# Kernel tuning notes

Hardware: AMD Instinct MI355X
Metric: run time of the kernel (lower is better)

Reference implementation:

```python
import jax, jax.numpy as jnp
import numpy as np

VOCAB, HID, L, HEADS, INTER, MAXSEQ, NCLS = 30522, 128, 2, 2, 512, 512, 2
HEAD = HID // HEADS
B, S = 128, 512


def _tlin(x, W, b):
    # TernaryLinear: threshold-quantize W to {-1,0,1} with per-tensor scale,
    # then ordinary linear. delta = 0.7*mean|W|, alpha = mean|W| over kept entries.
    absW = jnp.abs(W)
    delta = 0.7 * jnp.mean(absW)
    mask = (absW > delta).astype(W.dtype)
    alpha = jnp.sum(absW * mask) / jnp.maximum(jnp.sum(mask), 1.0)
    Wq = jnp.sign(W) * mask * alpha  # [out, in]
    return jnp.einsum('...i,oi->...o', x, Wq) + b


def _ln(x, g, b, eps=1e-5):
    m = jnp.mean(x, axis=-1, keepdims=True)
    v = jnp.var(x, axis=-1, keepdims=True)
    return (x - m) * jax.lax.rsqrt(v + eps) * g + b


def setup_inputs() -> dict:
    key = jax.random.key(0)
    ks = iter(jax.random.split(key, 64))
    n = lambda shape, s=0.02: jax.random.normal(next(ks), shape, dtype=jnp.float32) * s
    inp = {
        'input_ids': jax.random.randint(next(ks), (B, S), 0, VOCAB, dtype=jnp.int32).astype(jnp.int64),
        'tok_emb': n((VOCAB, HID)),
        'pos_emb': n((MAXSEQ, HID)),
        'ln_g': jnp.ones((HID,), jnp.float32), 'ln_b': jnp.zeros((HID,), jnp.float32),
        'qw': n((L, HID, HID)), 'qb': jnp.zeros((L, HID), jnp.float32),
        'kw': n((L, HID, HID)), 'kb': jnp.zeros((L, HID), jnp.float32),
        'vw': n((L, HID, HID)), 'vb': jnp.zeros((L, HID), jnp.float32),
        'aow': n((L, HID, HID)), 'aob': jnp.zeros((L, HID), jnp.float32),
        'iw': n((L, INTER, HID)), 'ib': jnp.zeros((L, INTER), jnp.float32),
        'fow': n((L, HID, INTER)), 'fob': jnp.zeros((L, HID), jnp.float32),
        'ln1g': jnp.ones((L, HID), jnp.float32), 'ln1b': jnp.zeros((L, HID), jnp.float32),
        'ln2g': jnp.ones((L, HID), jnp.float32), 'ln2b': jnp.zeros((L, HID), jnp.float32),
        'clf_w': n((NCLS, HID)), 'clf_b': jnp.zeros((NCLS,), jnp.float32),
    }
    return inp


def reference(input_ids, tok_emb, pos_emb, ln_g, ln_b, qw, qb, kw, kb, vw, vb,
              aow, aob, iw, ib, fow, fob, ln1g, ln1b, ln2g, ln2b, clf_w, clf_b):
    b, s = input_ids.shape
    x = tok_emb[input_ids] + pos_emb[jnp.arange(s)][None, :, :]  # [B,S,H]
    x = _ln(x, ln_g, ln_b)
    scale = 1.0 / (HEAD ** 0.5)
    for l in range(L):
        q = _tlin(x, qw[l], qb[l]).reshape(b, s, HEADS, HEAD)
        k = _tlin(x, kw[l], kb[l]).reshape(b, s, HEADS, HEAD)
        v = _tlin(x, vw[l], vb[l]).reshape(b, s, HEADS, HEAD)
        scores = jnp.einsum('bqhd,bkhd->bhqk', q, k) * scale
        attn = jax.nn.softmax(scores, axis=-1)
        ctx = jnp.einsum('bhqk,bkhd->bqhd', attn, v).reshape(b, s, HID)
        attn_out = _tlin(ctx, aow[l], aob[l])
        x = _ln(x + attn_out, ln1g[l], ln1b[l])
        ff = _tlin(jax.nn.relu(_tlin(x, iw[l], ib[l])), fow[l], fob[l])
        x = _ln(x + ff, ln2g[l], ln2b[l])
    cls = x[:, 0, :]
    logits = _tlin(cls, clf_w, clf_b)  # [B, NCLS]
    return logits
```

## Files before the change

### kernel.cpp

```cpp
#include <hip/hip_runtime.h>

typedef short bf8s __attribute__((ext_vector_type(8)));
typedef float f32x4 __attribute__((ext_vector_type(4)));

#define MFMA16(a, b, c) __builtin_amdgcn_mfma_f32_16x16x32_bf16(a, b, c, 0, 0, 0)

constexpr int S_ = 512, HID_ = 128, B_ = 128, M_ = B_ * S_;

__device__ inline short f2bf(float f) {
  unsigned u = __float_as_uint(f);
  u = (u + 0x7fffu + ((u >> 16) & 1u)) >> 16;
  return (short)u;
}
__device__ inline float bf2f(short s) {
  return __uint_as_float(((unsigned)(unsigned short)s) << 16);
}

__device__ inline float block_red1024(float v, float* red) {
  #pragma unroll
  for (int m = 32; m >= 1; m >>= 1) v += __shfl_xor(v, m);
  __syncthreads();
  if ((threadIdx.x & 63) == 0) red[threadIdx.x >> 6] = v;
  __syncthreads();
  float t = 0.f;
  #pragma unroll
  for (int i = 0; i < 16; ++i) t += red[i];
  return t;
}

__device__ inline void mat_info(int mat, const float* qw, const float* kw,
                                const float* vw, const float* aow, const float* iw,
                                const float* fw, const float* cw,
                                const float** src, int* n, int* doff) {
  if (mat < 6) {
    int l = mat / 3, which = mat % 3;
    const float* t[3] = {qw, kw, vw};
    *src = t[which] + l * 16384; *n = 16384; *doff = l * 49152 + which * 16384;
  } else if (mat < 8) {
    int l = mat - 6;
    *src = aow + l * 16384; *n = 16384; *doff = 98304 + l * 16384;
  } else if (mat < 10) {
    *src = iw + (mat - 8) * 65536; *n = 65536; *doff = 131072 + (mat - 8) * 65536;
  } else if (mat < 12) {
    *src = fw + (mat - 10) * 65536; *n = 65536; *doff = 262144 + (mat - 10) * 65536;
  } else {
    *src = cw; *n = 256; *doff = 393216;
  }
}

__global__ __launch_bounds__(1024) void k_qe(const float* qw, const float* kw,
    const float* vw, const float* aow, const float* iw, const float* fw,
    const float* cw, short* WQ,
    const int* __restrict__ ids, const float* __restrict__ tok,
    const float* __restrict__ pos, const float* __restrict__ g,
    const float* __restrict__ bb, short* xb) {
  __shared__ float red[16];
  int tid = threadIdx.x;
  if (blockIdx.x < 13) {
    const float* src; int n, doff;
    mat_info(blockIdx.x, qw, kw, vw, aow, iw, fw, cw, &src, &n, &doff);
    float s = 0.f;
    for (int i = tid; i < n; i += 1024) s += fabsf(src[i]);
    s = block_red1024(s, red);
    float delta = 0.7f * s / (float)n;
    float s2 = 0.f, c2 = 0.f;
    for (int i = tid; i < n; i += 1024) {
      float a = fabsf(src[i]);
      if (a > delta) { s2 += a; c2 += 1.f; }
    }
    s2 = block_red1024(s2, red);
    c2 = block_red1024(c2, red);
    float alpha = s2 / fmaxf(c2, 1.f);
    for (int i = tid; i < n; i += 1024) {
      float w = src[i];
      WQ[doff + i] = (fabsf(w) > delta) ? f2bf(w > 0.f ? alpha : -alpha) : (short)0;
    }
  } else {
    int wave = tid >> 6, lane = tid & 63;
    int t = (blockIdx.x - 13) * 16 + wave;
    int s = t & (S_ - 1);
    int id = ids[t];
    float e0 = tok[(size_t)id * HID_ + lane] + pos[(size_t)s * HID_ + lane];
    float e1 = tok[(size_t)id * HID_ + 64 + lane] + pos[(size_t)s * HID_ + 64 + lane];
    float sum = e0 + e1, ssq = e0 * e0 + e1 * e1;
    #pragma unroll
    for (int m = 32; m >= 1; m >>= 1) {
      sum += __shfl_xor(sum, m);
      ssq += __shfl_xor(ssq, m);
    }
    float mean = sum / 128.f;
    float var = ssq / 128.f - mean * mean;
    float rs = rsqrtf(var + 1e-5f);
    size_t o = (size_t)t * HID_;
    xb[o + lane]      = f2bf((e0 - mean) * rs * g[lane] + bb[lane]);
    xb[o + 64 + lane] = f2bf((e1 - mean) * rs * g[64 + lane] + bb[64 + lane]);
  }
}

__global__ __launch_bounds__(256) void k_qkv(
    const short* __restrict__ A, const short* __restrict__ W,
    const float* __restrict__ b0, const float* __restrict__ b1,
    const float* __restrict__ b2, short* outb) {
  __shared__ short Wl[128 * 136];
  int tid = threadIdx.x, lane = tid & 63, wave = tid >> 6;
  int row16 = lane & 15, quad = lane >> 4;
  int tok0 = blockIdx.x * 64 + wave * 16;
  int nbase = blockIdx.y * 128;

  const short* arow = A + (size_t)(tok0 + row16) * 128 + quad * 8;
  bf8s av[4];
  #pragma unroll
  for (int ki = 0; ki < 4; ++ki) av[ki] = *(const bf8s*)(arow + ki * 32);

  {
    int r = tid >> 1, half = tid & 1;
    const short* src = W + (size_t)(nbase + r) * 128 + half * 64;
    short* dst = &Wl[r * 136 + half * 64];
    #pragma unroll
    for (int j = 0; j < 8; ++j)
      *(bf8s*)(dst + j * 8) = *(const bf8s*)(src + j * 8);
  }
  __syncthreads();

  f32x4 acc[8] = {};
  #pragma unroll
  for (int ki = 0; ki < 4; ++ki)
    #pragma unroll
    for (int ot = 0; ot < 8; ++ot) {
      bf8s b = *(const bf8s*)(&Wl[(ot * 16 + row16) * 136 + ki * 32 + quad * 8]);
      acc[ot] = MFMA16(av[ki], b, acc[ot]);
    }

  const float* bp = (blockIdx.y == 0) ? b0 : ((blockIdx.y == 1) ? b1 : b2);
  float osc = (blockIdx.y == 0) ? 0.125f : 1.0f;
  int m0 = tok0 + quad * 4;
  #pragma unroll
  for (int ot = 0; ot < 8; ++ot) {
    int col = ot * 16 + row16;
    float bi = bp[col];
    #pragma unroll
    for (int r = 0; r < 4; ++r) {
      float v = (acc[ot][r] + bi) * osc;
      outb[(size_t)(m0 + r) * 384 + nbase + col] = f2bf(v);
    }
  }
}

__global__ __launch_bounds__(256) void k_aoff(
    const short* __restrict__ cb, const short* __restrict__ Wa,
    const float* __restrict__ aob, const float* __restrict__ ln1g,
    const float* __restrict__ ln1b, const short* __restrict__ Wi,
    const short* __restrict__ Wf, const float* __restrict__ ib,
    const float* __restrict__ fb, const float* __restrict__ ln2g,
    const float* __restrict__ ln2b, short* xb) {
  __shared__ short SM[22528];
  int tid = threadIdx.x, lane = tid & 63, wave = tid >> 6;
  int row16 = lane & 15, quad = lane >> 4;
  int tok0 = blockIdx.x * 64 + wave * 16;
  int m0 = tok0 + quad * 4;

  const short* arow = cb + (size_t)(tok0 + row16) * 128 + quad * 8;
  bf8s av[4];
  #pragma unroll
  for (int ki = 0; ki < 4; ++ki) av[ki] = *(const bf8s*)(arow + ki * 32);

  {
    int r = tid >> 1, half = tid & 1;
    const short* src = Wa + (size_t)r * 128 + half * 64;
    short* dst = &SM[r * 136 + half * 64];
    #pragma unroll
    for (int j = 0; j < 8; ++j)
      *(bf8s*)(dst + j * 8) = *(const bf8s*)(src + j * 8);
  }
  __syncthreads();

  f32x4 acc[8] = {};
  #pragma unroll
  for (int ki = 0; ki < 4; ++ki)
    #pragma unroll
    for (int ot = 0; ot < 8; ++ot) {
      bf8s b = *(const bf8s*)(&SM[(ot * 16 + row16) * 136 + ki * 32 + quad * 8]);
      acc[ot] = MFMA16(av[ki], b, acc[ot]);
    }

  int rwi = tid >> 2, q4 = tid & 3;
  int rwf = tid >> 1, hwf = tid & 1;
  const short* wisrc = Wi + (size_t)rwi * HID_ + q4 * 32;
  const short* wfsrc = Wf + (size_t)rwf * 512 + hwf * 32;
  bf8s wiR[4], wfR[4];
  #pragma unroll
  for (int j = 0; j < 4; ++j) {
    wiR[j] = *(const bf8s*)(wisrc + j * 8);
    wfR[j] = *(const bf8s*)(wfsrc + j * 8);
  }

  {
    float sum[4] = {}, ssq[4] = {};
    #pragma unroll
    for (int ot = 0; ot < 8; ++ot) {
      int col = ot * 16 + row16;
      float bi = aob[col];
      #pragma unroll
      for (int r = 0; r < 4; ++r) {
        float v = acc[ot][r] + bi + bf2f(xb[(size_t)(m0 + r) * HID_ + col]);
        acc[ot][r] = v;
        sum[r] += v; ssq[r] += v * v;
      }
    }
    #pragma unroll
    for (int m = 1; m <= 8; m <<= 1)
      #pragma unroll
      for (int r = 0; r < 4; ++r) {
        sum[r] += __shfl_xor(sum[r], m);
        ssq[r] += __shfl_xor(ssq[r], m);
      }
    float mean[4], rstd[4];
    #pragma unroll
    for (int r = 0; r < 4; ++r) {
      mean[r] = sum[r] / 128.f;
      float var = ssq[r] / 128.f - mean[r] * mean[r];
      rstd[r] = rsqrtf(var + 1e-5f);
    }
    #pragma unroll
    for (int ot = 0; ot < 8; ++ot) {
      int col = ot * 16 + row16;
      float gg = ln1g[col], bb2 = ln1b[col];
      #pragma unroll
      for (int r = 0; r < 4; ++r)
        acc[ot][r] = (acc[ot][r] - mean[r]) * rstd[r] * gg + bb2;
    }
  }

  #pragma unroll
  for (int ot = 0; ot < 8; ++ot) {
    int col = ot * 16 + row16;
    #pragma unroll
    for (int r = 0; r < 4; ++r)
      xb[(size_t)(m0 + r) * HID_ + col] = f2bf(acc[ot][r]);
  }

  __syncthreads();
  short* myX = &SM[wave * 4352];
  #pragma unroll
  for (int ot = 0; ot < 8; ++ot)
    #pragma unroll
    for (int r = 0; r < 4; ++r)
      myX[(quad * 4 + r) * 136 + ot * 16 + row16] = f2bf(acc[ot][r]);
  #pragma unroll
  for (int ki = 0; ki < 4; ++ki)
    av[ki] = *(const bf8s*)(myX + row16 * 136 + ki * 32 + quad * 8);

  short* SWi = SM;
  short* SWf = SM + 8704;
  short* mySt = SM + 17920 + wave * 1152;
  f32x4 acc2[8] = {};
  for (int c = 0; c < 8; ++c) {
    __syncthreads();
    {
      short* dwi = SWi + rwi * 136 + q4 * 32;
      short* dwf = SWf + rwf * 72 + hwf * 32;
      #pragma unroll
      for (int j = 0; j < 4; ++j) {
        *(bf8s*)(dwi + j * 8) = wiR[j];
        *(bf8s*)(dwf + j * 8) = wfR[j];
      }
    }
    __syncthreads();
    if (c < 7) {
      const short* ws1 = wisrc + (size_t)(c + 1) * 64 * HID_;
      const short* ws2 = wfsrc + (c + 1) * 64;
      #pragma unroll
      for (int j = 0; j < 4; ++j) {
        wiR[j] = *(const bf8s*)(ws1 + j * 8);
        wfR[j] = *(const bf8s*)(ws2 + j * 8);
      }
    }

    f32x4 hacc[4] = {};
    #pragma unroll
    for (int ki = 0; ki < 4; ++ki)
      #pragma unroll
      for (int ot = 0; ot < 4; ++ot) {
        bf8s b = *(const bf8s*)(SWi + (ot * 16 + row16) * 136 + ki * 32 + quad * 8);
        hacc[ot] = MFMA16(av[ki], b, hacc[ot]);
      }
    #pragma unroll
    for (int ot = 0; ot < 4; ++ot) {
      float bi = ib[c * 64 + ot * 16 + row16];
      #pragma unroll
      for (int r = 0; r < 4; ++r)
        mySt[(quad * 4 + r) * 72 + ot * 16 + row16] =
            f2bf(fmaxf(hacc[ot][r] + bi, 0.f));
    }
    bf8s ha0 = *(const bf8s*)(mySt + row16 * 72 + quad * 8);
    bf8s ha1 = *(const bf8s*)(mySt + row16 * 72 + 32 + quad * 8);
    #pragma unroll
    for (int ot = 0; ot < 8; ++ot) {
      bf8s bA = *(const bf8s*)(SWf + (ot * 16 + row16) * 72 + quad * 8);
      bf8s bB = *(const bf8s*)(SWf + (ot * 16 + row16) * 72 + 32 + quad * 8);
      acc2[ot] = MFMA16(ha0, bA, acc2[ot]);
      acc2[ot] = MFMA16(ha1, bB, acc2[ot]);
    }
  }

  float sum[4] = {}, ssq[4] = {};
  #pragma unroll
  for (int ot = 0; ot < 8; ++ot) {
    int col = ot * 16 + row16;
    float bi = fb[col];
    #pragma unroll
    for (int r = 0; r < 4; ++r) {
      float v = acc2[ot][r] + bi + bf2f(xb[(size_t)(m0 + r) * HID_ + col]);
      acc2[ot][r] = v;
      sum[r] += v; ssq[r] += v * v;
    }
  }
  #pragma unroll
  for (int m = 1; m <= 8; m <<= 1)
    #pragma unroll
    for (int r = 0; r < 4; ++r) {
      sum[r] += __shfl_xor(sum[r], m);
      ssq[r] += __shfl_xor(ssq[r], m);
    }
  float mean[4], rstd[4];
  #pragma unroll
  for (int r = 0; r < 4; ++r) {
    mean[r] = sum[r] / 128.f;
    float var = ssq[r] / 128.f - mean[r] * mean[r];
    rstd[r] = rsqrtf(var + 1e-5f);
  }
  #pragma unroll
  for (int ot = 0; ot < 8; ++ot) {
    int col = ot * 16 + row16;
    float gg = ln2g[col], bb2 = ln2b[col];
    #pragma unroll
    for (int r = 0; r < 4; ++r) {
      float v = (acc2[ot][r] - mean[r]) * rstd[r] * gg + bb2;
      xb[(size_t)(m0 + r) * HID_ + col] = f2bf(v);
    }
  }
}

__global__ __launch_bounds__(512) void k_attn(const short* __restrict__ qkv,
                                              short* __restrict__ O) {
  __shared__ short Kl[64 * 72];
  __shared__ short Vtl[64 * 72];
  __shared__ short Pl[8][16 * 72];

  int tid = threadIdx.x, lane = tid & 63, wave = tid >> 6;
  int row16 = lane & 15, quad = lane >> 4;
  int b = blockIdx.x >> 2, h = (blockIdx.x >> 1) & 1, qhalf = blockIdx.x & 1;
  const short* base  = qkv + (size_t)b * S_ * 384;
  const short* kbase = base + 128 + h * 64;
  const short* vbase = base + 256 + h * 64;
  int q0 = qhalf * 256 + wave * 32;

  bf8s qa[2][2];
  #pragma unroll
  for (int qf = 0; qf < 2; ++qf) {
    const short* qrow = base + h * 64 +
        (size_t)(q0 + qf * 16 + row16) * 384 + quad * 8;
    qa[qf][0] = *(const bf8s*)(qrow);
    qa[qf][1] = *(const bf8s*)(qrow + 32);
  }

  int krow = tid >> 3, dgk = tid & 7;
  int vkey = tid & 63, dgv = tid >> 6;
  const short* kptr = kbase + (size_t)krow * 384 + dgk * 8;
  const short* vptr = vbase + (size_t)vkey * 384 + dgv * 8;
  bf8s kst = *(const bf8s*)(kptr);
  bf8s vst = *(const bf8s*)(vptr);

  float li[2][4] = {};
  f32x4 oacc[2][4] = {};
  short* myP = &Pl[wave][0];

  for (int kt0 = 0; kt0 < S_; kt0 += 64) {
    if (kt0) __syncthreads();
    *(bf8s*)(&Kl[krow * 72 + dgk * 8]) = kst;
    #pragma unroll
    for (int j = 0; j < 8; ++j) Vtl[(dgv * 8 + j) * 72 + vkey] = vst[j];
    __syncthreads();
    if (kt0 + 64 < S_) {
      kst = *(const bf8s*)(kptr + (size_t)(kt0 + 64) * 384);
      vst = *(const bf8s*)(vptr + (size_t)(kt0 + 64) * 384);
    }

    f32x4 sc[2][4] = {};
    #pragma unroll
    for (int ks = 0; ks < 4; ++ks) {
      const short* kp = &Kl[(ks * 16 + row16) * 72 + quad * 8];
      bf8s k0 = *(const bf8s*)(kp);
      bf8s k1 = *(const bf8s*)(kp + 32);
      sc[0][ks] = MFMA16(qa[0][0], k0, sc[0][ks]);
      sc[0][ks] = MFMA16(qa[0][1], k1, sc[0][ks]);
      sc[1][ks] = MFMA16(qa[1][0], k0, sc[1][ks]);
      sc[1][ks] = MFMA16(qa[1][1], k1, sc[1][ks]);
    }

    #pragma unroll
    for (int qf = 0; qf < 2; ++qf) {
      #pragma unroll
      for (int ks = 0; ks < 4; ++ks)
        #pragma unroll
        for (int r = 0; r < 4; ++r) {
          float pv = __expf(sc[qf][ks][r]);
          li[qf][r] += pv;
          myP[(quad * 4 + r) * 72 + ks * 16 + row16] = f2bf(pv);
        }
      bf8s pa0 = *(const bf8s*)(&myP[row16 * 72 + quad * 8]);
      bf8s pa1 = *(const bf8s*)(&myP[row16 * 72 + 32 + quad * 8]);
      #pragma unroll
      for (int dt = 0; dt < 4; ++dt) {
        const short* vp = &Vtl[(dt * 16 + row16) * 72 + quad * 8];
        bf8s v0 = *(const bf8s*)(vp);
        bf8s v1 = *(const bf8s*)(vp + 32);
        oacc[qf][dt] = MFMA16(pa0, v0, oacc[qf][dt]);
        oacc[qf][dt] = MFMA16(pa1, v1, oacc[qf][dt]);
      }
    }
  }

  #pragma unroll
  for (int qf = 0; qf < 2; ++qf) {
    float inv[4];
    #pragma unroll
    for (int r = 0; r < 4; ++r) {
      float t = li[qf][r];
      #pragma unroll
      for (int m = 1; m <= 8; m <<= 1) t += __shfl_xor(t, m);
      inv[r] = 1.f / t;
    }
    size_t trow = (size_t)(b * S_ + q0 + qf * 16 + quad * 4);
    #pragma unroll
    for (int dt = 0; dt < 4; ++dt)
      #pragma unroll
      for (int r = 0; r < 4; ++r)
        O[(trow + r) * HID_ + h * 64 + dt * 16 + row16] =
            f2bf(oacc[qf][dt][r] * inv[r]);
  }
}

__global__ __launch_bounds__(256) void k_clf(const short* __restrict__ xb,
    const short* __restrict__ Wc, const float* __restrict__ cbias, float* out) {
  int i = threadIdx.x;
  int b = i >> 1, c = i & 1;
  float s = 0.f;
  for (int k = 0; k < HID_; ++k)
    s += bf2f(xb[(size_t)b * S_ * HID_ + k]) * bf2f(Wc[c * HID_ + k]);
  out[b * 2 + c] = s + cbias[c];
}

extern "C" void kernel_launch(void* const* d_in, const int* in_sizes, int n_in,
                              void* d_out, int out_size, void* d_ws, size_t ws_size,
                              hipStream_t stream) {
  const int*   ids     = (const int*)d_in[0];
  const float* tok_emb = (const float*)d_in[1];
  const float* pos_emb = (const float*)d_in[2];
  const float* ln_g    = (const float*)d_in[3];
  const float* ln_bb   = (const float*)d_in[4];
  const float* qw      = (const float*)d_in[5];
  const float* qbias   = (const float*)d_in[6];
  const float* kw      = (const float*)d_in[7];
  const float* kbias   = (const float*)d_in[8];
  const float* vw      = (const float*)d_in[9];
  const float* vbias   = (const float*)d_in[10];
  const float* aow     = (const float*)d_in[11];
  const float* aobias  = (const float*)d_in[12];
  const float* iw      = (const float*)d_in[13];
  const float* ibias   = (const float*)d_in[14];
  const float* fow     = (const float*)d_in[15];
  const float* fbias   = (const float*)d_in[16];
  const float* ln1g    = (const float*)d_in[17];
  const float* ln1b    = (const float*)d_in[18];
  const float* ln2g    = (const float*)d_in[19];
  const float* ln2b    = (const float*)d_in[20];
  const float* clfw    = (const float*)d_in[21];
  const float* clfb    = (const float*)d_in[22];

  char* ws = (char*)d_ws;
  short* WQ  = (short*)ws;
  short* xb  = (short*)(ws + 1048576);
  short* qkv = (short*)(ws + 1048576 + 16777216);
  short* cb_ = qkv + (size_t)M_ * 384;

  k_qe<<<13 + M_ / 16, 1024, 0, stream>>>(qw, kw, vw, aow, iw, fow, clfw, WQ,
                                          ids, tok_emb, pos_emb, ln_g, ln_bb, xb);

  for (int l = 0; l < 2; ++l) {
    const short* Wqkv = WQ + (size_t)l * 49152;
    const short* Wa   = WQ + 98304 + (size_t)l * 16384;
    const short* Wi   = WQ + 131072 + (size_t)l * 65536;
    const short* Wf   = WQ + 262144 + (size_t)l * 65536;

    k_qkv<<<dim3(M_ / 64, 3), 256, 0, stream>>>(
        xb, Wqkv, qbias + l * HID_, kbias + l * HID_, vbias + l * HID_, qkv);
    k_attn<<<512, 512, 0, stream>>>(qkv, cb_);
    k_aoff<<<M_ / 64, 256, 0, stream>>>(
        cb_, Wa, aobias + l * HID_, ln1g + l * HID_, ln1b + l * HID_,
        Wi, Wf, ibias + l * 512, fbias + l * HID_,
        ln2g + l * HID_, ln2b + l * HID_, xb);
  }

  k_clf<<<1, 256, 0, stream>>>(xb, WQ + 393216, clfb, (float*)d_out);
}
```

Before: 355.4 us.

## Fuse layer-1 QKV projection into layer-0 FFN kernel; use 128-token blocks

The layer-0 attention-output/FFN kernel now also computes the layer-1 QKV projection from its LayerNorm output, which removes one k_qkv launch and one re-read of the hidden state from global memory. Blocks now cover 128 tokens with 512 threads, so each weight tile staged in LDS is shared by twice as many tokens. The LDS row pitch changes from 136 to 144 (and 72 to 80), altering the bank-conflict pattern. In exchange, LDS use per block is higher and the fused kernel holds more registers, which may lower occupancy.

```diff
diff --git a/kernel.cpp b/kernel.cpp
--- a/kernel.cpp
+++ b/kernel.cpp
@@ -101,7 +101,7 @@
     const short* __restrict__ A, const short* __restrict__ W,
     const float* __restrict__ b0, const float* __restrict__ b1,
     const float* __restrict__ b2, short* outb) {
-  __shared__ short Wl[128 * 136];
+  __shared__ short Wl[128 * 144];
   int tid = threadIdx.x, lane = tid & 63, wave = tid >> 6;
   int row16 = lane & 15, quad = lane >> 4;
   int tok0 = blockIdx.x * 64 + wave * 16;
@@ -115,7 +115,7 @@
   {
     int r = tid >> 1, half = tid & 1;
     const short* src = W + (size_t)(nbase + r) * 128 + half * 64;
-    short* dst = &Wl[r * 136 + half * 64];
+    short* dst = &Wl[r * 144 + half * 64];
     #pragma unroll
     for (int j = 0; j < 8; ++j)
       *(bf8s*)(dst + j * 8) = *(const bf8s*)(src + j * 8);
@@ -127,7 +127,7 @@
   for (int ki = 0; ki < 4; ++ki)
     #pragma unroll
     for (int ot = 0; ot < 8; ++ot) {
-      bf8s b = *(const bf8s*)(&Wl[(ot * 16 + row16) * 136 + ki * 32 + quad * 8]);
+      bf8s b = *(const bf8s*)(&Wl[(ot * 16 + row16) * 144 + ki * 32 + quad * 8]);
       acc[ot] = MFMA16(av[ki], b, acc[ot]);
     }
 
@@ -146,17 +146,21 @@
   }
 }
 
-__global__ __launch_bounds__(256) void k_aoff(
+template <int DOQKV>
+__global__ __launch_bounds__(512) void k_aoff(
     const short* __restrict__ cb, const short* __restrict__ Wa,
     const float* __restrict__ aob, const float* __restrict__ ln1g,
     const float* __restrict__ ln1b, const short* __restrict__ Wi,
     const short* __restrict__ Wf, const float* __restrict__ ib,
     const float* __restrict__ fb, const float* __restrict__ ln2g,
-    const float* __restrict__ ln2b, short* xb) {
-  __shared__ short SM[22528];
+    const float* __restrict__ ln2b, short* xb,
+    const short* __restrict__ Wqkv2, const float* __restrict__ qb2,
+    const float* __restrict__ kb2, const float* __restrict__ vb2,
+    short* qkvout) {
+  __shared__ short SM[29696];
   int tid = threadIdx.x, lane = tid & 63, wave = tid >> 6;
   int row16 = lane & 15, quad = lane >> 4;
-  int tok0 = blockIdx.x * 64 + wave * 16;
+  int tok0 = blockIdx.x * 128 + wave * 16;
   int m0 = tok0 + quad * 4;
 
   const short* arow = cb + (size_t)(tok0 + row16) * 128 + quad * 8;
@@ -165,11 +169,11 @@
   for (int ki = 0; ki < 4; ++ki) av[ki] = *(const bf8s*)(arow + ki * 32);
 
   {
-    int r = tid >> 1, half = tid & 1;
-    const short* src = Wa + (size_t)r * 128 + half * 64;
-    short* dst = &SM[r * 136 + half * 64];
-    #pragma unroll
-    for (int j = 0; j < 8; ++j)
+    int r = tid >> 2, q4 = tid & 3;
+    const short* src = Wa + (size_t)r * 128 + q4 * 32;
+    short* dst = &SM[r * 144 + q4 * 32];
+    #pragma unroll
+    for (int j = 0; j < 4; ++j)
       *(bf8s*)(dst + j * 8) = *(const bf8s*)(src + j * 8);
   }
   __syncthreads();
@@ -179,17 +183,17 @@
   for (int ki = 0; ki < 4; ++ki)
     #pragma unroll
     for (int ot = 0; ot < 8; ++ot) {
-      bf8s b = *(const bf8s*)(&SM[(ot * 16 + row16) * 136 + ki * 32 + quad * 8]);
+      bf8s b = *(const bf8s*)(&SM[(ot * 16 + row16) * 144 + ki * 32 + quad * 8]);
       acc[ot] = MFMA16(av[ki], b, acc[ot]);
     }
 
-  int rwi = tid >> 2, q4 = tid & 3;
-  int rwf = tid >> 1, hwf = tid & 1;
-  const short* wisrc = Wi + (size_t)rwi * HID_ + q4 * 32;
-  const short* wfsrc = Wf + (size_t)rwf * 512 + hwf * 32;
-  bf8s wiR[4], wfR[4];
-  #pragma unroll
-  for (int j = 0; j < 4; ++j) {
+  int rwi = tid >> 3, q8 = tid & 7;
+  int rwf = tid >> 2, qf4 = tid & 3;
+  const short* wisrc = Wi + (size_t)rwi * HID_ + q8 * 16;
+  const short* wfsrc = Wf + (size_t)rwf * 512 + qf4 * 16;
+  bf8s wiR[2], wfR[2];
+  #pragma unroll
+  for (int j = 0; j < 2; ++j) {
     wiR[j] = *(const bf8s*)(wisrc + j * 8);
     wfR[j] = *(const bf8s*)(wfsrc + j * 8);
   }
@@ -240,27 +244,29 @@
   }
 
   __syncthreads();
-  short* myX = &SM[wave * 4352];
-  #pragma unroll
-  for (int ot = 0; ot < 8; ++ot)
-    #pragma unroll
-    for (int r = 0; r < 4; ++r)
-      myX[(quad * 4 + r) * 136 + ot * 16 + row16] = f2bf(acc[ot][r]);
-  #pragma unroll
-  for (int ki = 0; ki < 4; ++ki)
-    av[ki] = *(const bf8s*)(myX + row16 * 136 + ki * 32 + quad * 8);
+  {
+    short* myX = &SM[wave * 2304];
+    #pragma unroll
+    for (int ot = 0; ot < 8; ++ot)
+      #pragma unroll
+      for (int r = 0; r < 4; ++r)
+        myX[(quad * 4 + r) * 144 + ot * 16 + row16] = f2bf(acc[ot][r]);
+    #pragma unroll
+    for (int ki = 0; ki < 4; ++ki)
+      av[ki] = *(const bf8s*)(myX + row16 * 144 + ki * 32 + quad * 8);
+  }
 
   short* SWi = SM;
-  short* SWf = SM + 8704;
-  short* mySt = SM + 17920 + wave * 1152;
+  short* SWf = SM + 9216;
+  short* mySt = SM + 19456 + wave * 1280;
   f32x4 acc2[8] = {};
   for (int c = 0; c < 8; ++c) {
     __syncthreads();
     {
-      short* dwi = SWi + rwi * 136 + q4 * 32;
-      short* dwf = SWf + rwf * 72 + hwf * 32;
-      #pragma unroll
-      for (int j = 0; j < 4; ++j) {
+      short* dwi = SWi + rwi * 144 + q8 * 16;
+      short* dwf = SWf + rwf * 80 + qf4 * 16;
+      #pragma unroll
+      for (int j = 0; j < 2; ++j) {
         *(bf8s*)(dwi + j * 8) = wiR[j];
         *(bf8s*)(dwf + j * 8) = wfR[j];
       }
@@ -270,7 +276,7 @@
       const short* ws1 = wisrc + (size_t)(c + 1) * 64 * HID_;
       const short* ws2 = wfsrc + (c + 1) * 64;
       #pragma unroll
-      for (int j = 0; j < 4; ++j) {
+      for (int j = 0; j < 2; ++j) {
         wiR[j] = *(const bf8s*)(ws1 + j * 8);
         wfR[j] = *(const bf8s*)(ws2 + j * 8);
       }
@@ -281,7 +287,7 @@
     for (int ki = 0; ki < 4; ++ki)
       #pragma unroll
       for (int ot = 0; ot < 4; ++ot) {
-        bf8s b = *(const bf8s*)(SWi + (ot * 16 + row16) * 136 + ki * 32 + quad * 8);
+        bf8s b = *(const bf8s*)(SWi + (ot * 16 + row16) * 144 + ki * 32 + quad * 8);
         hacc[ot] = MFMA16(av[ki], b, hacc[ot]);
       }
     #pragma unroll
@@ -289,54 +295,105 @@
       float bi = ib[c * 64 + ot * 16 + row16];
       #pragma unroll
       for (int r = 0; r < 4; ++r)
-        mySt[(quad * 4 + r) * 72 + ot * 16 + row16] =
+        mySt[(quad * 4 + r) * 80 + ot * 16 + row16] =
             f2bf(fmaxf(hacc[ot][r] + bi, 0.f));
     }
-    bf8s ha0 = *(const bf8s*)(mySt + row16 * 72 + quad * 8);
-    bf8s ha1 = *(const bf8s*)(mySt + row16 * 72 + 32 + quad * 8);
-    #pragma unroll
-    for (int ot = 0; ot < 8; ++ot) {
-      bf8s bA = *(const bf8s*)(SWf + (ot * 16 + row16) * 72 + quad * 8);
-      bf8s bB = *(const bf8s*)(SWf + (ot * 16 + row16) * 72 + 32 + quad * 8);
+    bf8s ha0 = *(const bf8s*)(mySt + row16 * 80 + quad * 8);
+    bf8s ha1 = *(const bf8s*)(mySt + row16 * 80 + 32 + quad * 8);
+    #pragma unroll
+    for (int ot = 0; ot < 8; ++ot) {
+      bf8s bA = *(const bf8s*)(SWf + (ot * 16 + row16) * 80 + quad * 8);
+      bf8s bB = *(const bf8s*)(SWf + (ot * 16 + row16) * 80 + 32 + quad * 8);
       acc2[ot] = MFMA16(ha0, bA, acc2[ot]);
       acc2[ot] = MFMA16(ha1, bB, acc2[ot]);
     }
   }
 
-  float sum[4] = {}, ssq[4] = {};
-  #pragma unroll
-  for (int ot = 0; ot < 8; ++ot) {
-    int col = ot * 16 + row16;
-    float bi = fb[col];
+  {
+    float sum[4] = {}, ssq[4] = {};
+    #pragma unroll
+    for (int ot = 0; ot < 8; ++ot) {
+      int col = ot * 16 + row16;
+      float bi = fb[col];
+      #pragma unroll
+      for (int r = 0; r < 4; ++r) {
+        float v = acc2[ot][r] + bi + bf2f(xb[(size_t)(m0 + r) * HID_ + col]);
+        acc2[ot][r] = v;
+        sum[r] += v; ssq[r] += v * v;
+      }
+    }
+    #pragma unroll
+    for (int m = 1; m <= 8; m <<= 1)
+      #pragma unroll
+      for (int r = 0; r < 4; ++r) {
+        sum[r] += __shfl_xor(sum[r], m);
+        ssq[r] += __shfl_xor(ssq[r], m);
+      }
+    float mean[4], rstd[4];
     #pragma unroll
     for (int r = 0; r < 4; ++r) {
-      float v = acc2[ot][r] + bi + bf2f(xb[(size_t)(m0 + r) * HID_ + col]);
-      acc2[ot][r] = v;
-      sum[r] += v; ssq[r] += v * v;
-    }
-  }
-  #pragma unroll
-  for (int m = 1; m <= 8; m <<= 1)
-    #pragma unroll
-    for (int r = 0; r < 4; ++r) {
-      sum[r] += __shfl_xor(sum[r], m);
-      ssq[r] += __shfl_xor(ssq[r], m);
-    }
-  float mean[4], rstd[4];
-  #pragma unroll
-  for (int r = 0; r < 4; ++r) {
-    mean[r] = sum[r] / 128.f;
-    float var = ssq[r] / 128.f - mean[r] * mean[r];
-    rstd[r] = rsqrtf(var + 1e-5f);
-  }
-  #pragma unroll
-  for (int ot = 0; ot < 8; ++ot) {
-    int col = ot * 16 + row16;
-    float gg = ln2g[col], bb2 = ln2b[col];
-    #pragma unroll
-    for (int r = 0; r < 4; ++r) {
-      float v = (acc2[ot][r] - mean[r]) * rstd[r] * gg + bb2;
-      xb[(size_t)(m0 + r) * HID_ + col] = f2bf(v);
+      mean[r] = sum[r] / 128.f;
+      float var = ssq[r] / 128.f - mean[r] * mean[r];
+      rstd[r] = rsqrtf(var + 1e-5f);
+    }
+    #pragma unroll
+    for (int ot = 0; ot < 8; ++ot) {
+      int col = ot * 16 + row16;
+      float gg = ln2g[col], bb2 = ln2b[col];
+      #pragma unroll
+      for (int r = 0; r < 4; ++r) {
+        float v = (acc2[ot][r] - mean[r]) * rstd[r] * gg + bb2;
+        acc2[ot][r] = v;
+        xb[(size_t)(m0 + r) * HID_ + col] = f2bf(v);
+      }
+    }
+  }
+
+  if (DOQKV) {
+    __syncthreads();
+    bf8s av2[4];
+    {
+      short* myX = &SM[wave * 2304];
+      #pragma unroll
+      for (int ot = 0; ot < 8; ++ot)
+        #pragma unroll
+        for (int r = 0; r < 4; ++r)
+          myX[(quad * 4 + r) * 144 + ot * 16 + row16] = f2bf(acc2[ot][r]);
+      #pragma unroll
+      for (int ki = 0; ki < 4; ++ki)
+        av2[ki] = *(const bf8s*)(myX + row16 * 144 + ki * 32 + quad * 8);
+    }
+    for (int c3 = 0; c3 < 3; ++c3) {
+      __syncthreads();
+      {
+        int r = tid >> 2, q4 = tid & 3;
+        const short* src = Wqkv2 + (size_t)(c3 * 128 + r) * 128 + q4 * 32;
+        short* dst = &SM[r * 144 + q4 * 32];
+        #pragma unroll
+        for (int j = 0; j < 4; ++j)
+          *(bf8s*)(dst + j * 8) = *(const bf8s*)(src + j * 8);
+      }
+      __syncthreads();
+      f32x4 acc3[8] = {};
+      #pragma unroll
+      for (int ki = 0; ki < 4; ++ki)
+        #pragma unroll
+        for (int ot = 0; ot < 8; ++ot) {
+          bf8s b = *(const bf8s*)(&SM[(ot * 16 + row16) * 144 + ki * 32 + quad * 8]);
+          acc3[ot] = MFMA16(av2[ki], b, acc3[ot]);
+        }
+      const float* bp = (c3 == 0) ? qb2 : ((c3 == 1) ? kb2 : vb2);
+      float osc = (c3 == 0) ? 0.125f : 1.0f;
+      #pragma unroll
+      for (int ot = 0; ot < 8; ++ot) {
+        int col = ot * 16 + row16;
+        float bi = bp[col];
+        #pragma unroll
+        for (int r = 0; r < 4; ++r) {
+          float v = (acc3[ot][r] + bi) * osc;
+          qkvout[(size_t)(m0 + r) * 384 + c3 * 128 + col] = f2bf(v);
+        }
+      }
     }
   }
 }
@@ -487,20 +544,26 @@
   k_qe<<<13 + M_ / 16, 1024, 0, stream>>>(qw, kw, vw, aow, iw, fow, clfw, WQ,
                                           ids, tok_emb, pos_emb, ln_g, ln_bb, xb);
 
-  for (int l = 0; l < 2; ++l) {
-    const short* Wqkv = WQ + (size_t)l * 49152;
-    const short* Wa   = WQ + 98304 + (size_t)l * 16384;
-    const short* Wi   = WQ + 131072 + (size_t)l * 65536;
-    const short* Wf   = WQ + 262144 + (size_t)l * 65536;
-
-    k_qkv<<<dim3(M_ / 64, 3), 256, 0, stream>>>(
-        xb, Wqkv, qbias + l * HID_, kbias + l * HID_, vbias + l * HID_, qkv);
-    k_attn<<<512, 512, 0, stream>>>(qkv, cb_);
-    k_aoff<<<M_ / 64, 256, 0, stream>>>(
-        cb_, Wa, aobias + l * HID_, ln1g + l * HID_, ln1b + l * HID_,
-        Wi, Wf, ibias + l * 512, fbias + l * HID_,
-        ln2g + l * HID_, ln2b + l * HID_, xb);
-  }
+  const short* Wqkv0 = WQ;
+  const short* Wqkv1 = WQ + 49152;
+  const short* Wa0   = WQ + 98304;
+  const short* Wa1   = WQ + 98304 + 16384;
+  const short* Wi0   = WQ + 131072;
+  const short* Wi1   = WQ + 131072 + 65536;
+  const short* Wf0   = WQ + 262144;
+  const short* Wf1   = WQ + 262144 + 65536;
+
+  k_qkv<<<dim3(M_ / 64, 3), 256, 0, stream>>>(
+      xb, Wqkv0, qbias, kbias, vbias, qkv);
+  k_attn<<<512, 512, 0, stream>>>(qkv, cb_);
+  k_aoff<1><<<M_ / 128, 512, 0, stream>>>(
+      cb_, Wa0, aobias, ln1g, ln1b, Wi0, Wf0, ibias, fbias, ln2g, ln2b, xb,
+      Wqkv1, qbias + HID_, kbias + HID_, vbias + HID_, qkv);
+  k_attn<<<512, 512, 0, stream>>>(qkv, cb_);
+  k_aoff<0><<<M_ / 128, 512, 0, stream>>>(
+      cb_, Wa1, aobias + HID_, ln1g + HID_, ln1b + HID_, Wi1, Wf1,
+      ibias + 512, fbias + HID_, ln2g + HID_, ln2b + HID_, xb,
+      nullptr, nullptr, nullptr, nullptr, nullptr);
 
   k_clf<<<1, 256, 0, stream>>>(xb, WQ + 393216, clfb, (float*)d_out);
 }
```

Result: faster. 328.7 us (-7.5%).
